# Kernel tuning notes

Hardware: AMD Instinct MI355X
Metric: run time of the kernel (lower is better)

Reference implementation:

```python
import jax, jax.numpy as jnp
import numpy as np

B, D, H, DEPTH = 1024, 1024, 1024, 4


def setup_inputs() -> dict:
    key = jax.random.key(0)
    k_x, k_w, k_ws, k_bs = jax.random.split(key, 4)
    x = jax.random.normal(k_x, (B, D), dtype=jnp.float32)
    W_enc = jax.random.normal(k_w, (D, H), dtype=jnp.float32) * 0.02
    b_enc = jnp.zeros((H,), dtype=jnp.float32)
    # per-layer CrossNet weights, matching keras random_normal init (stddev=0.05)
    ws = jax.random.normal(k_ws, (DEPTH, H, 1), dtype=jnp.float32) * 0.05
    bs = jax.random.normal(k_bs, (DEPTH, H, 1), dtype=jnp.float32) * 0.05
    return {"x": x, "W_enc": W_enc, "b_enc": b_enc, "ws": ws, "bs": bs}


def reference(x, W_enc, b_enc, ws, bs):
    # encoder Dense
    h = jnp.matmul(x, W_enc) + b_enc  # (B, H)
    x0 = h
    x_l = h
    depth = ws.shape[0]
    for l in range(depth):
        # original: (x0[:, :, None] * x_l[:, None, :]) @ w + b, squeezed.
        # outer[b,i,j] @ w  == x0[b,i] * sum_j x_l[b,j] * w[j]
        s = jnp.matmul(x_l, ws[l])            # (B, 1)
        residual = x0 * s + bs[l][:, 0]       # (B, H)
        x_l = residual + x_l
    return x_l
```

## Files before the change

### kernel.cpp

```cpp
#include <hip/hip_runtime.h>
#include <hip/hip_bf16.h>


#define B_SZ 1024
#define D_SZ 1024
#define H_SZ 1024
#define DEPTH 4

typedef _Float16 half4_t __attribute__((ext_vector_type(4)));
typedef _Float16 half8_t __attribute__((ext_vector_type(8)));
typedef float float16_t __attribute__((ext_vector_type(16)));

typedef const __attribute__((address_space(1))) unsigned int* gas_ptr;
typedef __attribute__((address_space(3))) unsigned int* las_ptr;

__device__ __forceinline__ void async_copy16(const void* g, void* l) {
    __builtin_amdgcn_global_load_lds((gas_ptr)g, (las_ptr)l, 16, 0, 0);
}

__global__ __launch_bounds__(256) void prep_kernel(
        const float* __restrict__ x, const float* __restrict__ W,
        _Float16* __restrict__ xh, _Float16* __restrict__ Wt) {
    const int b = blockIdx.x;
    const int t = threadIdx.x;
    if (b < 256) {
        __shared__ float S[64][65];
        const int k0 = (b >> 4) << 6;
        const int n0 = (b & 15) << 6;
#pragma unroll
        for (int i = 0; i < 4; ++i) {
            int idx = (i << 8) + t;
            int r = idx >> 4;
            int c4 = idx & 15;
            float4 v = *(const float4*)(W + (size_t)(k0 + r) * H_SZ + n0 + (c4 << 2));
            S[r][(c4 << 2) + 0] = v.x;
            S[r][(c4 << 2) + 1] = v.y;
            S[r][(c4 << 2) + 2] = v.z;
            S[r][(c4 << 2) + 3] = v.w;
        }
        __syncthreads();
#pragma unroll
        for (int i = 0; i < 4; ++i) {
            int idx = (i << 8) + t;
            int n = idx >> 4;
            int c4 = idx & 15;
            int k = c4 << 2;
            half4_t o;
            o.x = (_Float16)S[k + 0][n];
            o.y = (_Float16)S[k + 1][n];
            o.z = (_Float16)S[k + 2][n];
            o.w = (_Float16)S[k + 3][n];
            *(half4_t*)(Wt + (size_t)(n0 + n) * D_SZ + k0 + k) = o;
        }
    } else {
        const int base = (b - 256) * 4096;
#pragma unroll
        for (int i = 0; i < 4; ++i) {
            int off = base + (((i << 8) + t) << 2);
            float4 v = *(const float4*)(x + off);
            half4_t o;
            o.x = (_Float16)v.x; o.y = (_Float16)v.y;
            o.z = (_Float16)v.z; o.w = (_Float16)v.w;
            *(half4_t*)(xh + off) = o;
        }
    }
}

__global__ __launch_bounds__(256) void gemm_kernel(
        const _Float16* __restrict__ xh, const _Float16* __restrict__ Wt,
        float* __restrict__ h) {
    __shared__ _Float16 As[64 * 32];
    __shared__ _Float16 Bs[64 * 32];
    const int tid  = threadIdx.x;
    const int w    = tid >> 6;
    const int lane = tid & 63;
    const int m0 = blockIdx.y << 6;
    const int n0 = blockIdx.x << 6;
    const int wm = (w >> 1) << 5;
    const int wn = (w & 1) << 5;

    const int srow = tid >> 2;
    const int scol = (tid & 3) << 3;
    const _Float16* aSrc = xh + (size_t)(m0 + srow) * D_SZ + scol;
    const _Float16* bSrc = Wt + (size_t)(n0 + srow) * D_SZ + scol;
    _Float16* aDst = As + (w << 9);
    _Float16* bDst = Bs + (w << 9);

    const int arow = wm + (lane & 31);
    const int brow = wn + (lane & 31);
    const int koff = (lane >> 5) << 3;

    float16_t acc;
#pragma unroll
    for (int i = 0; i < 16; ++i) acc[i] = 0.0f;

    for (int k0 = 0; k0 < D_SZ; k0 += 32) {
        async_copy16(aSrc + k0, aDst);
        async_copy16(bSrc + k0, bDst);
        __syncthreads();
#pragma unroll
        for (int kc = 0; kc < 32; kc += 16) {
            half8_t af = *(const half8_t*)(As + arow * 32 + kc + koff);
            half8_t bf = *(const half8_t*)(Bs + brow * 32 + kc + koff);
            acc = __builtin_amdgcn_mfma_f32_32x32x16_f16(af, bf, acc, 0, 0, 0);
        }
        __syncthreads();
    }

    const int col = n0 + wn + (lane & 31);
    const int rbase = m0 + wm + ((lane >> 5) << 2);
#pragma unroll
    for (int r = 0; r < 16; ++r) {
        int row = rbase + (r & 3) + ((r >> 2) << 3);
        h[(size_t)row * H_SZ + col] = acc[r];
    }
}

__global__ __launch_bounds__(256) void crossnet_kernel(
        float* __restrict__ h, const float* __restrict__ b_enc,
        const float* __restrict__ ws, const float* __restrict__ bs) {
    const int row = blockIdx.x;
    const int t = threadIdx.x;
    float* hr = h + (size_t)row * H_SZ;

    float4 hv = *(const float4*)(hr + (t << 2));
    float4 be = *(const float4*)(b_enc + (t << 2));
    float x0[4] = {hv.x + be.x, hv.y + be.y, hv.z + be.z, hv.w + be.w};
    float xl[4] = {x0[0], x0[1], x0[2], x0[3]};

    __shared__ float red[4];
    __shared__ float sbc;

    for (int l = 0; l < DEPTH; ++l) {
        float4 wv = *(const float4*)(ws + l * H_SZ + (t << 2));
        float4 bv = *(const float4*)(bs + l * H_SZ + (t << 2));
        float p = xl[0] * wv.x + xl[1] * wv.y + xl[2] * wv.z + xl[3] * wv.w;
#pragma unroll
        for (int off = 32; off > 0; off >>= 1) p += __shfl_down(p, off, 64);
        if ((t & 63) == 0) red[t >> 6] = p;
        __syncthreads();
        if (t == 0) sbc = red[0] + red[1] + red[2] + red[3];
        __syncthreads();
        float s = sbc;
        xl[0] += x0[0] * s + bv.x;
        xl[1] += x0[1] * s + bv.y;
        xl[2] += x0[2] * s + bv.z;
        xl[3] += x0[3] * s + bv.w;
    }
    float4 o = {xl[0], xl[1], xl[2], xl[3]};
    *(float4*)(hr + (t << 2)) = o;
}

extern "C" void kernel_launch(void* const* d_in, const int* in_sizes, int n_in,
                              void* d_out, int out_size, void* d_ws, size_t ws_size,
                              hipStream_t stream) {
    const float* x     = (const float*)d_in[0];
    const float* W_enc = (const float*)d_in[1];
    const float* b_enc = (const float*)d_in[2];
    const float* ws    = (const float*)d_in[3];
    const float* bs    = (const float*)d_in[4];
    float* out = (float*)d_out;

    _Float16* xh = (_Float16*)d_ws;
    _Float16* Wt = xh + (size_t)B_SZ * D_SZ;

    prep_kernel<<<512, 256, 0, stream>>>(x, W_enc, xh, Wt);
    dim3 grid(H_SZ / 64, B_SZ / 64);
    gemm_kernel<<<grid, 256, 0, stream>>>(xh, Wt, out);
    crossnet_kernel<<<B_SZ, 256, 0, stream>>>(out, b_enc, ws, bs);
}
```

Baseline: 87.58 us.

## Double-buffer GEMM with swizzled LDS, 16x16 MFMA, and streamline crossnet reduction

The GEMM now uses 32x64 output tiles with 512 threads and a K-step of 64. Tiles are double-buffered in LDS, so the async global-to-LDS copy of the next step overlaps the MFMA work on the current one, with a single barrier per iteration. An XOR swizzle on LDS columns avoids bank conflicts, and each wave runs 16x16x32 MFMAs on its own 16x16 sub-tile. The crossnet kernel preloads all layer weights and biases and drops the second barrier by having every thread sum the per-layer partials itself, at the cost of more registers and LDS slots per layer.

Result: faster. 82.76 us (-5.5%).

```diff
diff --git a/kernel.cpp b/kernel.cpp
--- a/kernel.cpp
+++ b/kernel.cpp
@@ -9,7 +9,7 @@
 
 typedef _Float16 half4_t __attribute__((ext_vector_type(4)));
 typedef _Float16 half8_t __attribute__((ext_vector_type(8)));
-typedef float float16_t __attribute__((ext_vector_type(16)));
+typedef float floatx4_t __attribute__((ext_vector_type(4)));
 
 typedef const __attribute__((address_space(1))) unsigned int* gas_ptr;
 typedef __attribute__((address_space(3))) unsigned int* las_ptr;
@@ -66,54 +66,57 @@
     }
 }
 
-__global__ __launch_bounds__(256) void gemm_kernel(
+__global__ __launch_bounds__(512) void gemm_kernel(
         const _Float16* __restrict__ xh, const _Float16* __restrict__ Wt,
         float* __restrict__ h) {
-    __shared__ _Float16 As[64 * 32];
-    __shared__ _Float16 Bs[64 * 32];
+    __shared__ _Float16 As[2][32 * 64];
+    __shared__ _Float16 Bs[2][64 * 64];
     const int tid  = threadIdx.x;
+    const int lane = tid & 63;
     const int w    = tid >> 6;
-    const int lane = tid & 63;
-    const int m0 = blockIdx.y << 6;
+    const int m0 = blockIdx.y << 5;
     const int n0 = blockIdx.x << 6;
-    const int wm = (w >> 1) << 5;
-    const int wn = (w & 1) << 5;
+    const int wm = (w >> 2) << 4;
+    const int wn = (w & 3) << 4;
 
-    const int srow = tid >> 2;
-    const int scol = (tid & 3) << 3;
-    const _Float16* aSrc = xh + (size_t)(m0 + srow) * D_SZ + scol;
-    const _Float16* bSrc = Wt + (size_t)(n0 + srow) * D_SZ + scol;
-    _Float16* aDst = As + (w << 9);
-    _Float16* bDst = Bs + (w << 9);
+    const int sr = tid >> 3;
+    const int sc = ((tid & 7) ^ (sr & 7)) << 3;
+    const _Float16* aSrc = xh + (size_t)(m0 + (sr & 31)) * D_SZ + sc;
+    const _Float16* bSrc = Wt + (size_t)(n0 + sr) * D_SZ + sc;
 
-    const int arow = wm + (lane & 31);
-    const int brow = wn + (lane & 31);
-    const int koff = (lane >> 5) << 3;
+    const int ra = wm + (lane & 15);
+    const int rb = wn + (lane & 15);
+    const int q  = lane >> 4;
 
-    float16_t acc;
+    floatx4_t acc = {0.0f, 0.0f, 0.0f, 0.0f};
+
+    if (tid < 256) async_copy16(aSrc, &As[0][tid << 3]);
+    async_copy16(bSrc, &Bs[0][tid << 3]);
+
+    for (int it = 0; it < 16; ++it) {
+        __syncthreads();
+        if (it + 1 < 16) {
+            int k0 = (it + 1) << 6;
+            int buf = (it + 1) & 1;
+            if (tid < 256) async_copy16(aSrc + k0, &As[buf][tid << 3]);
+            async_copy16(bSrc + k0, &Bs[buf][tid << 3]);
+        }
+        const _Float16* Ab = As[it & 1];
+        const _Float16* Bb = Bs[it & 1];
 #pragma unroll
-    for (int i = 0; i < 16; ++i) acc[i] = 0.0f;
-
-    for (int k0 = 0; k0 < D_SZ; k0 += 32) {
-        async_copy16(aSrc + k0, aDst);
-        async_copy16(bSrc + k0, bDst);
-        __syncthreads();
-#pragma unroll
-        for (int kc = 0; kc < 32; kc += 16) {
-            half8_t af = *(const half8_t*)(As + arow * 32 + kc + koff);
-            half8_t bf = *(const half8_t*)(Bs + brow * 32 + kc + koff);
-            acc = __builtin_amdgcn_mfma_f32_32x32x16_f16(af, bf, acc, 0, 0, 0);
+        for (int kk = 0; kk < 2; ++kk) {
+            int l = (kk << 2) + q;
+            half8_t af = *(const half8_t*)(Ab + ra * 64 + ((l ^ (ra & 7)) << 3));
+            half8_t bf = *(const half8_t*)(Bb + rb * 64 + ((l ^ (rb & 7)) << 3));
+            acc = __builtin_amdgcn_mfma_f32_16x16x32_f16(af, bf, acc, 0, 0, 0);
         }
-        __syncthreads();
     }
 
-    const int col = n0 + wn + (lane & 31);
-    const int rbase = m0 + wm + ((lane >> 5) << 2);
+    const int col = n0 + wn + (lane & 15);
+    const int row0 = m0 + wm + (q << 2);
 #pragma unroll
-    for (int r = 0; r < 16; ++r) {
-        int row = rbase + (r & 3) + ((r >> 2) << 3);
-        h[(size_t)row * H_SZ + col] = acc[r];
-    }
+    for (int r = 0; r < 4; ++r)
+        h[(size_t)(row0 + r) * H_SZ + col] = acc[r];
 }
 
 __global__ __launch_bounds__(256) void crossnet_kernel(
@@ -125,27 +128,29 @@
 
     float4 hv = *(const float4*)(hr + (t << 2));
     float4 be = *(const float4*)(b_enc + (t << 2));
+    float4 wv[DEPTH], bv[DEPTH];
+#pragma unroll
+    for (int l = 0; l < DEPTH; ++l) {
+        wv[l] = *(const float4*)(ws + l * H_SZ + (t << 2));
+        bv[l] = *(const float4*)(bs + l * H_SZ + (t << 2));
+    }
     float x0[4] = {hv.x + be.x, hv.y + be.y, hv.z + be.z, hv.w + be.w};
     float xl[4] = {x0[0], x0[1], x0[2], x0[3]};
 
-    __shared__ float red[4];
-    __shared__ float sbc;
+    __shared__ float red[DEPTH][4];
 
+#pragma unroll
     for (int l = 0; l < DEPTH; ++l) {
-        float4 wv = *(const float4*)(ws + l * H_SZ + (t << 2));
-        float4 bv = *(const float4*)(bs + l * H_SZ + (t << 2));
-        float p = xl[0] * wv.x + xl[1] * wv.y + xl[2] * wv.z + xl[3] * wv.w;
+        float p = xl[0] * wv[l].x + xl[1] * wv[l].y + xl[2] * wv[l].z + xl[3] * wv[l].w;
 #pragma unroll
         for (int off = 32; off > 0; off >>= 1) p += __shfl_down(p, off, 64);
-        if ((t & 63) == 0) red[t >> 6] = p;
+        if ((t & 63) == 0) red[l][t >> 6] = p;
         __syncthreads();
-        if (t == 0) sbc = red[0] + red[1] + red[2] + red[3];
-        __syncthreads();
-        float s = sbc;
-        xl[0] += x0[0] * s + bv.x;
-        xl[1] += x0[1] * s + bv.y;
-        xl[2] += x0[2] * s + bv.z;
-        xl[3] += x0[3] * s + bv.w;
+        float s = red[l][0] + red[l][1] + red[l][2] + red[l][3];
+        xl[0] += x0[0] * s + bv[l].x;
+        xl[1] += x0[1] * s + bv[l].y;
+        xl[2] += x0[2] * s + bv[l].z;
+        xl[3] += x0[3] * s + bv[l].w;
     }
     float4 o = {xl[0], xl[1], xl[2], xl[3]};
     *(float4*)(hr + (t << 2)) = o;
@@ -165,7 +170,7 @@
     _Float16* Wt = xh + (size_t)B_SZ * D_SZ;
 
     prep_kernel<<<512, 256, 0, stream>>>(x, W_enc, xh, Wt);
-    dim3 grid(H_SZ / 64, B_SZ / 64);
-    gemm_kernel<<<grid, 256, 0, stream>>>(xh, Wt, out);
+    dim3 grid(H_SZ / 64, B_SZ / 32);
+    gemm_kernel<<<grid, 512, 0, stream>>>(xh, Wt, out);
     crossnet_kernel<<<B_SZ, 256, 0, stream>>>(out, b_enc, ws, bs);
 }
```
